# Performance work log

Hardware: AMD Instinct MI355X
Metric: run time of the kernel (lower is better)

Reference implementation:

```python
import jax, jax.numpy as jnp
import numpy as np

E, R, D, H = 8, 16, 2048, 8192
B, S = 2, 2048
SCALING = 2.0  # lora_alpha / r = 32 / 16


def gelu_new(x):
    # HF ACT2FN['gelu_new'] (tanh approximation), matches Phi config
    c = np.sqrt(2.0 / np.pi).astype(np.float32)
    return 0.5 * x * (1.0 + jnp.tanh(c * (x + 0.044715 * x * x * x)))


def _moe_lora(x, onehot, A, Bm):
    # x: [T,Din], A: [E,R,Din], Bm: [E,Dout,R], onehot: [T,E]
    # per-token low-rank projection for every expert (R is tiny), mask to the
    # assigned expert, then contract (e,r) jointly -> single [T,E*R]@[E*R,Dout] GEMM
    z = jnp.einsum('td,erd->ter', x, A) * onehot[:, :, None]  # [T,E,R]
    return jnp.einsum('ter,ehr->th', z, Bm)                   # [T,Dout]


def setup_inputs() -> dict:
    key = jax.random.key(0)
    ks = jax.random.split(key, 10)
    inv = lambda n: np.float32(1.0 / np.sqrt(n))
    return {
        'hidden_states': jax.random.normal(ks[0], (B, S, D), jnp.float32),
        'expert_idx': jax.random.randint(ks[1], (B, S), 0, E),
        'W1': jax.random.normal(ks[2], (H, D), jnp.float32) * inv(D),
        'b1': jax.random.normal(ks[3], (H,), jnp.float32) * 0.02,
        'A1': jax.random.normal(ks[4], (E, R, D), jnp.float32) * inv(D),
        'B1': jax.random.normal(ks[5], (E, H, R), jnp.float32) * 0.02,
        'W2': jax.random.normal(ks[6], (D, H), jnp.float32) * inv(H),
        'b2': jax.random.normal(ks[7], (D,), jnp.float32) * 0.02,
        'A2': jax.random.normal(ks[8], (E, R, H), jnp.float32) * inv(H),
        'B2': jax.random.normal(ks[9], (E, D, R), jnp.float32) * 0.02,
    }


def reference(hidden_states, expert_idx, W1, b1, A1, B1, W2, b2, A2, B2):
    b, s, d = hidden_states.shape
    x = hidden_states.reshape(b * s, d)                       # [T,D]
    onehot = jax.nn.one_hot(expert_idx.reshape(-1), A1.shape[0], dtype=x.dtype)
    # expert fc1: shared base layer + per-expert LoRA + shared bias
    h1 = x @ W1.T + b1 + SCALING * _moe_lora(x, onehot, A1, B1)
    y = gelu_new(h1)                                          # [T,H]
    # expert fc2
    out = y @ W2.T + b2 + SCALING * _moe_lora(y, onehot, A2, B2)
    return out.reshape(b, s, d)
```

## Files before the change

kernel.cpp:

```cpp
#include <hip/hip_runtime.h>
#include <hip/hip_bf16.h>
#include <math.h>

typedef __bf16 bf16_t;
typedef __bf16 bf16x4_t __attribute__((ext_vector_type(4)));
typedef __bf16 bf16x8_t __attribute__((ext_vector_type(8)));
typedef float  f32x4    __attribute__((ext_vector_type(4)));

#define NE  8
#define NR  16
#define ND  2048
#define NH  8192
#define NT  4096
#define NER 128
#define NK1 (ND + NER)
#define NK2 (NH + NER)

static __device__ __forceinline__ float gelu_fast(float x) {
    const float c2 = 1.5957691216057308f;
    float u2 = c2 * (x + 0.044715f * x * x * x);
    return x / (1.0f + __expf(-u2));
}

static __device__ __forceinline__ void load16_to_lds(const bf16_t* g, bf16_t* l) {
    __builtin_amdgcn_global_load_lds(
        (__attribute__((address_space(1))) void*)(g),
        (__attribute__((address_space(3))) void*)(l),
        16, 0, 0);
}

__global__ __launch_bounds__(256) void conv_x(
    const float* __restrict__ x, bf16_t* __restrict__ Xa1)
{
    const int i  = blockIdx.x * 256 + threadIdx.x;
    const int row = i >> 8;
    const int c8  = i & 255;
    f32x4 v0 = *(const f32x4*)(x + (long)i * 8);
    f32x4 v1 = *(const f32x4*)(x + (long)i * 8 + 4);
    bf16x8_t o = {(bf16_t)v0[0], (bf16_t)v0[1], (bf16_t)v0[2], (bf16_t)v0[3],
                  (bf16_t)v1[0], (bf16_t)v1[1], (bf16_t)v1[2], (bf16_t)v1[3]};
    *(bf16x8_t*)(Xa1 + (long)row * NK1 + (c8 << 3)) = o;
}

__global__ __launch_bounds__(256) void prep_main(
    const float* __restrict__ W, bf16_t* __restrict__ Waug,
    int ld, int shift8, int total8)
{
    const int i = blockIdx.x * 256 + threadIdx.x;
    if (i >= total8) return;
    const int row = i >> shift8;
    const int c8  = i & ((1 << shift8) - 1);
    f32x4 v0 = *(const f32x4*)(W + (long)i * 8);
    f32x4 v1 = *(const f32x4*)(W + (long)i * 8 + 4);
    bf16x8_t o = {(bf16_t)v0[0], (bf16_t)v0[1], (bf16_t)v0[2], (bf16_t)v0[3],
                  (bf16_t)v1[0], (bf16_t)v1[1], (bf16_t)v1[2], (bf16_t)v1[3]};
    *(bf16x8_t*)(Waug + (long)row * ld + (c8 << 3)) = o;
}

__global__ __launch_bounds__(256) void prep_lora(
    const float* __restrict__ Bl, bf16_t* __restrict__ Waug,
    int nrows, int K0, int ld, int total)
{
    const int i = blockIdx.x * 256 + threadIdx.x;
    if (i >= total) return;
    const int row = i >> 7;
    const int c   = i & 127;
    const int e   = c >> 4;
    const int r   = c & 15;
    float v = Bl[((long)e * nrows + row) * NR + r];
    Waug[(long)row * ld + K0 + c] = (bf16_t)v;
}

template <int SPLITS, int LD>
__global__ __launch_bounds__(256) void zred(
    const float* __restrict__ zp, const int* __restrict__ eidx,
    bf16_t* __restrict__ dst)
{
    const int i = blockIdx.x * 256 + threadIdx.x;
    const int t = i >> 7;
    const int c = i & 127;
    float s = 0.f;
#pragma unroll
    for (int j = 0; j < SPLITS; ++j) s += zp[(long)j * NT * 128 + i];
    const int e = eidx[t];
    float v = ((c >> 4) == e) ? 2.0f * s : 0.f;
    dst[(long)t * LD + c] = (bf16_t)v;
}

template <int BM, int BN, int W, int WM, int WN,
          int K, int LDA, int LDB, int LDC, int MODE>
__global__ __launch_bounds__(W * 64) void gemm_bt(
    const bf16_t* __restrict__ A,  const bf16_t* __restrict__ Bt,
    const float* __restrict__ bias, void* __restrict__ Cout)
{
    constexpr int RW  = BM / WM;
    constexpr int CW  = BN / WN;
    constexpr int MT  = RW / 16;
    constexpr int NTn = CW / 16;
    constexpr int AI  = BM / 16 / W;
    constexpr int BI  = BN / 16 / W;

    __shared__ union {
        struct { bf16_t As[2 * BM * 32]; bf16_t Bs[2 * BN * 32]; } s;
        bf16_t Cs[64 * 264];
    } u;

    const int tid   = threadIdx.x;
    const int wave  = tid >> 6;
    const int lane  = tid & 63;
    const int col16 = lane & 15;
    const int q     = lane >> 4;
    const int wm    = wave % WM;
    const int wn    = wave / WM;

    const int  rowA0 = blockIdx.y * BM;
    const int  colB0 = (MODE == 3) ? 0 : blockIdx.x * BN;
    const long koff  = (MODE == 3) ? (long)blockIdx.x * K : 0;

    const int srow  = lane >> 2;
    const int skoff = (lane & 3) * 8;

    const bf16_t* Agp[AI][2];
    const bf16_t* Bgp[BI][2];
    bf16_t*       AsD[AI][2];
    bf16_t*       BsD[BI][2];
#pragma unroll
    for (int jj = 0; jj < AI; ++jj) {
        const int j = (wave + jj * W) * 16;
#pragma unroll
        for (int h = 0; h < 2; ++h) {
            Agp[jj][h] = A + (long)(rowA0 + j + srow) * LDA + koff + h * 32 + skoff;
            AsD[jj][h] = &u.s.As[(h * BM + j) * 32];
        }
    }
#pragma unroll
    for (int jj = 0; jj < BI; ++jj) {
        const int j = (wave + jj * W) * 16;
#pragma unroll
        for (int h = 0; h < 2; ++h) {
            Bgp[jj][h] = Bt + (long)(colB0 + j + srow) * LDB + koff + h * 32 + skoff;
            BsD[jj][h] = &u.s.Bs[(h * BN + j) * 32];
        }
    }

    const bf16_t* Ard = &u.s.As[(wm * RW + col16) * 32 + q * 8];
    const bf16_t* Brd = &u.s.Bs[(wn * CW + col16) * 32 + q * 8];

    f32x4 acc[MT][NTn];
#pragma unroll
    for (int i = 0; i < MT; ++i)
#pragma unroll
        for (int j = 0; j < NTn; ++j)
            acc[i][j] = (f32x4){0.f, 0.f, 0.f, 0.f};

    for (int it = 0; it < K / 64; ++it) {
#pragma unroll
        for (int jj = 0; jj < AI; ++jj)
#pragma unroll
            for (int h = 0; h < 2; ++h) {
                load16_to_lds(Agp[jj][h], AsD[jj][h]);
                Agp[jj][h] += 64;
            }
#pragma unroll
        for (int jj = 0; jj < BI; ++jj)
#pragma unroll
            for (int h = 0; h < 2; ++h) {
                load16_to_lds(Bgp[jj][h], BsD[jj][h]);
                Bgp[jj][h] += 64;
            }
        __syncthreads();

#pragma unroll
        for (int h = 0; h < 2; ++h) {
            bf16x8_t af[MT], bfr[NTn];
#pragma unroll
            for (int mt = 0; mt < MT; ++mt)
                af[mt] = *(const bf16x8_t*)(Ard + (h * BM + mt * 16) * 32);
#pragma unroll
            for (int nt = 0; nt < NTn; ++nt)
                bfr[nt] = *(const bf16x8_t*)(Brd + (h * BN + nt * 16) * 32);
#pragma unroll
            for (int mt = 0; mt < MT; ++mt)
#pragma unroll
                for (int nt = 0; nt < NTn; ++nt)
                    acc[mt][nt] = __builtin_amdgcn_mfma_f32_16x16x32_bf16(
                        af[mt], bfr[nt], acc[mt][nt], 0, 0, 0);
        }
        __syncthreads();
    }

    if (MODE == 3) {
        float* Cf = (float*)Cout + (long)blockIdx.x * NT * LDC;
#pragma unroll
        for (int nt = 0; nt < NTn; ++nt) {
            const int col = wn * CW + nt * 16 + col16;
#pragma unroll
            for (int mt = 0; mt < MT; ++mt) {
                const int row0 = rowA0 + wm * RW + mt * 16 + q * 4;
#pragma unroll
                for (int i = 0; i < 4; ++i)
                    Cf[(long)(row0 + i) * LDC + col] = acc[mt][nt][i];
            }
        }
    }
}


#define BARRIER8() do { __builtin_amdgcn_sched_barrier(0); \
    __builtin_amdgcn_s_barrier(); \
    __builtin_amdgcn_sched_barrier(0); } while (0)

#define WAITLG8() do { asm volatile("s_waitcnt lgkmcnt(0)" ::: "memory"); \
    __builtin_amdgcn_sched_barrier(0); } while (0)

template <int N>
static __device__ __forceinline__ void wait_vm() {
    static_assert(N == 0 || N == 3 || N == 4, "unsupported vmcnt");
    if constexpr (N == 0) asm volatile("s_waitcnt vmcnt(0)" ::: "memory");
    if constexpr (N == 3) asm volatile("s_waitcnt vmcnt(3)" ::: "memory");
    if constexpr (N == 4) asm volatile("s_waitcnt vmcnt(4)" ::: "memory");
}

#define STAGE_A8(TT, KH) do { \
    char* ld_ = smem + (((((TT) & 1) << 1) + (KH)) * ASLOT) + sdW; \
    const bf16_t* g_ = gA + (long)(TT) * 64 + (KH) * 32; \
    _Pragma("unroll") \
    for (int j_ = 0; j_ < LA; ++j_) \
        load16_to_lds(g_ + (long)j_ * 128 * LDA_, (bf16_t*)(ld_ + j_ * 8192)); \
} while (0)

#define STAGE_B8(TT, KH) do { \
    char* ld_ = smem + BOFF0 + (((((TT) & 1) << 1) + (KH)) * BSLOT) + sdW; \
    const bf16_t* g_ = gB + (long)(TT) * 64 + (KH) * 32; \
    _Pragma("unroll") \
    for (int j_ = 0; j_ < LB; ++j_) \
        load16_to_lds(g_ + (long)j_ * 128 * LDB_, (bf16_t*)(ld_ + j_ * 8192)); \
} while (0)

#define RD_A8(RP, KH, MH) do { \
    const char* p_ = smem + (((RP) * 2 + (KH)) * ASLOT) \
                   + (wm * RW + (MH) * (RW / 2)) * 64 + rdoff; \
    _Pragma("unroll") \
    for (int mt_ = 0; mt_ < MT2; ++mt_) \
        af[mt_] = *(const bf16x8_t*)(p_ + mt_ * 1024); \
} while (0)

#define RD_B8(RP, KH) do { \
    const char* p_ = smem + BOFF0 + (((RP) * 2 + (KH)) * BSLOT) \
                   + (wn * CW) * 64 + rdoff; \
    _Pragma("unroll") \
    for (int nt_ = 0; nt_ < NTn; ++nt_) \
        bfr[nt_] = *(const bf16x8_t*)(p_ + nt_ * 1024); \
} while (0)

#define MFMA_PH8(MH) do { \
    __builtin_amdgcn_s_setprio(1); \
    _Pragma("unroll") \
    for (int mt_ = 0; mt_ < MT2; ++mt_) \
        _Pragma("unroll") \
        for (int nt_ = 0; nt_ < NTn; ++nt_) \
            acc[(MH) * MT2 + mt_][nt_] = __builtin_amdgcn_mfma_f32_16x16x32_bf16( \
                af[mt_], bfr[nt_], acc[(MH) * MT2 + mt_][nt_], 0, 0, 0); \
    __builtin_amdgcn_s_setprio(0); \
} while (0)

#define TILE8(T_, ST_) do { \
    const int rp_ = (T_) & 1; \
     \
    RD_A8(rp_, 0, 0); RD_B8(rp_, 0); \
    if (ST_) STAGE_A8((T_) + 1, 0); \
    BARRIER8(); WAITLG8(); MFMA_PH8(0); BARRIER8(); \
     \
    RD_A8(rp_, 0, 1); \
    if (ST_) { STAGE_B8((T_) + 1, 0); wait_vm<LA + LB>(); } \
    else     { wait_vm<0>(); } \
    BARRIER8(); WAITLG8(); MFMA_PH8(1); BARRIER8(); \
     \
    RD_A8(rp_, 1, 0); RD_B8(rp_, 1); \
    if (ST_) STAGE_A8((T_) + 1, 1); \
    BARRIER8(); WAITLG8(); MFMA_PH8(0); BARRIER8(); \
     \
    RD_A8(rp_, 1, 1); \
    if (ST_) { STAGE_B8((T_) + 1, 1); wait_vm<LA + LB>(); } \
    BARRIER8(); WAITLG8(); MFMA_PH8(1); BARRIER8(); \
} while (0)

template <int BN, int WM, int WN, int KT, int LDA_, int LDB_, int LDC_, int MODE>
__global__ __launch_bounds__(512, 2) void gemm8(
    const bf16_t* __restrict__ A, const bf16_t* __restrict__ Bt,
    const float* __restrict__ bias, void* __restrict__ Cout)
{
    constexpr int BM    = 256;
    constexpr int RW    = BM / WM;
    constexpr int CW    = BN / WN;
    constexpr int MT    = RW / 16;
    constexpr int MT2   = MT / 2;
    constexpr int NTn   = CW / 16;
    constexpr int LA    = 2;
    constexpr int LB    = BN / 128;
    constexpr int NTIL  = KT / 64;
    constexpr int ASLOT = 16384;
    constexpr int BSLOT = BN * 64;
    constexpr int BOFF0 = 4 * ASLOT;
    constexpr int RING  = BOFF0 + 4 * BSLOT;
    constexpr int CSB   = 64 * 264 * 2;
    constexpr int SMEM  = (MODE == 0 && CSB > RING) ? CSB : RING;

    __shared__ __align__(16) char smem[SMEM];

    const int tid   = threadIdx.x;
    const int wave  = tid >> 6;
    const int lane  = tid & 63;
    const int col16 = lane & 15;
    const int q     = lane >> 4;
    const int wm    = wave % WM;
    const int wn    = wave / WM;

    const int rowA0 = blockIdx.y * BM;
    const int colB0 = blockIdx.x * BN;

    const int srow = tid >> 2;
    const int sseg = (tid & 3) ^ ((tid >> 3) & 3);
    const bf16_t* gA = A  + (long)(rowA0 + srow) * LDA_ + sseg * 8;
    const bf16_t* gB = Bt + (long)(colB0 + srow) * LDB_ + sseg * 8;
    const int sdW = wave << 10;

    const int rdoff = col16 * 64 + ((q ^ ((lane >> 1) & 3)) << 4);

    bf16x8_t af[MT2];
    bf16x8_t bfr[NTn];
    f32x4 acc[MT][NTn];
#pragma unroll
    for (int i = 0; i < MT; ++i)
#pragma unroll
        for (int j = 0; j < NTn; ++j)
            acc[i][j] = (f32x4){0.f, 0.f, 0.f, 0.f};

    STAGE_A8(0, 0); STAGE_B8(0, 0); STAGE_A8(0, 1); STAGE_B8(0, 1);
    wait_vm<LA + LB>();
    BARRIER8();

    for (int t = 0; t < NTIL - 1; ++t) TILE8(t, 1);
    TILE8(NTIL - 1, 0);

    if (MODE == 1) {
        float* Cf = (float*)Cout;
#pragma unroll
        for (int nt = 0; nt < NTn; ++nt) {
            const int col = colB0 + wn * CW + nt * 16 + col16;
            const float bv = bias[col];
#pragma unroll
            for (int mt = 0; mt < MT; ++mt) {
                const int row0 = rowA0 + wm * RW + mt * 16 + q * 4;
#pragma unroll
                for (int i = 0; i < 4; ++i)
                    Cf[(long)(row0 + i) * LDC_ + col] = acc[mt][nt][i] + bv;
            }
        }
    } else {
        bf16_t* Cb = (bf16_t*)Cout;
        bf16_t* Cs = (bf16_t*)smem;
#pragma unroll
        for (int ph = 0; ph < BM / 64; ++ph) {
            const int phwm = (ph * 64) / RW;
            const int mtb  = ((ph * 64) % RW) / 16;
            if (wm == phwm) {
#pragma unroll
                for (int nt = 0; nt < NTn; ++nt) {
                    const int c = wn * CW + nt * 16 + col16;
                    const float bv = bias[colB0 + c];
#pragma unroll
                    for (int mt = 0; mt < 4; ++mt) {
                        const int rl = mt * 16 + q * 4;
#pragma unroll
                        for (int i = 0; i < 4; ++i)
                            Cs[(rl + i) * 264 + c] =
                                (bf16_t)gelu_fast(acc[mtb + mt][nt][i] + bv);
                    }
                }
            }
            __syncthreads();
            {
                constexpr int CPR = BN / 32;
                const int r  = tid / CPR;
                const int c0 = (tid % CPR) * 32;
                const long gbase =
                    (long)(rowA0 + ph * 64 + r) * LDC_ + colB0 + c0;
#pragma unroll
                for (int ch = 0; ch < 4; ++ch) {
                    bf16x8_t v = *(const bf16x8_t*)&Cs[r * 264 + c0 + ch * 8];
                    *(bf16x8_t*)&Cb[gbase + ch * 8] = v;
                }
            }
            __syncthreads();
        }
    }
}

extern "C" void kernel_launch(void* const* d_in, const int* in_sizes, int n_in,
                              void* d_out, int out_size, void* d_ws, size_t ws_size,
                              hipStream_t stream)
{
    const float* x    = (const float*)d_in[0];
    const int*   eidx = (const int*)  d_in[1];
    const float* W1   = (const float*)d_in[2];
    const float* b1   = (const float*)d_in[3];
    const float* A1   = (const float*)d_in[4];
    const float* B1   = (const float*)d_in[5];
    const float* W2   = (const float*)d_in[6];
    const float* b2   = (const float*)d_in[7];
    const float* A2   = (const float*)d_in[8];
    const float* B2   = (const float*)d_in[9];
    float* out = (float*)d_out;

    char* ws = (char*)d_ws;
    bf16_t* Xaug2 = (bf16_t*)(ws);
    bf16_t* Xaug1 = (bf16_t*)(ws + 68157440L);
    bf16_t* W1aug = (bf16_t*)(ws + 85983232L);
    bf16_t* W2aug = (bf16_t*)(ws + 68157440L);
    bf16_t* A1b   = (bf16_t*)(ws + 104000000L);
    bf16_t* A2b   = (bf16_t*)(ws + 104857600L);
    float*  zp1   = (float*) (ws + 106954752L);
    float*  zp2   = (float*) (ws + 85983232L);

    conv_x<<<NT * ND / 8 / 256, 256, 0, stream>>>(x, Xaug1);
    prep_main<<<(NER * ND / 8) / 256, 256, 0, stream>>>(A1, A1b, ND, 8, NER * ND / 8);
    {
        dim3 g(4, NT / 128);
        gemm_bt<128, 128, 4, 2, 2, 512, NK1, ND, 128, 3><<<g, 256, 0, stream>>>(
            Xaug1, A1b, nullptr, (void*)zp1);
    }
    zred<4, NK1><<<NT * 128 / 256, 256, 0, stream>>>(zp1, eidx, Xaug1 + ND);
    prep_main<<<(NH * ND / 8) / 256, 256, 0, stream>>>(W1, W1aug, NK1, 8, NH * ND / 8);
    prep_lora<<<(NH * NER) / 256, 256, 0, stream>>>(B1, W1aug, NH, ND, NK1, NH * NER);
    {
        dim3 g(NH / 256, NT / 256);
        gemm8<256, 2, 4, NK1, NK1, NK1, NK2, 0><<<g, 512, 0, stream>>>(
            Xaug1, W1aug, b1, (void*)Xaug2);
    }

    prep_main<<<(NER * NH / 8) / 256, 256, 0, stream>>>(A2, A2b, NH, 10, NER * NH / 8);
    {
        dim3 g(8, NT / 128);
        gemm_bt<128, 128, 4, 2, 2, 1024, NK2, NH, 128, 3><<<g, 256, 0, stream>>>(
            Xaug2, A2b, nullptr, (void*)zp2);
    }
    zred<8, NK2><<<NT * 128 / 256, 256, 0, stream>>>(zp2, eidx, Xaug2 + NH);
    prep_main<<<(ND * NH / 8) / 256, 256, 0, stream>>>(W2, W2aug, NK2, 10, ND * NH / 8);
    prep_lora<<<(ND * NER) / 256, 256, 0, stream>>>(B2, W2aug, ND, NH, NK2, ND * NER);
    {
        dim3 g(ND / 128, NT / 256);
        gemm8<128, 4, 2, NK2, NK2, NK2, ND, 1><<<g, 512, 0, stream>>>(
            Xaug2, W2aug, b2, (void*)out);
    }
}
```

Baseline: 550.9 us.

## Deepen GEMM K-pipeline prefetch and use inline-asm LDS reads with immediate offsets

Restructures the staged global-to-LDS pipeline so that parts of tile t+2 are prefetched while tile t is computed. Only the second A half of tile t+1 is left for the current iteration, and the vmcnt waits and prologue are adjusted to match. LDS fragment reads become explicit ds_read_b128 with immediate offsets, which cuts address arithmetic. The aim is to hide more global-load latency behind the MFMA work. In exchange it relies on slot reuse across the 2-deep ring being correct, and asm volatile reads may limit the compiler's scheduling.

```diff
diff --git a/kernel.cpp b/kernel.cpp
--- a/kernel.cpp
+++ b/kernel.cpp
@@ -6,6 +6,7 @@
 typedef __bf16 bf16x4_t __attribute__((ext_vector_type(4)));
 typedef __bf16 bf16x8_t __attribute__((ext_vector_type(8)));
 typedef float  f32x4    __attribute__((ext_vector_type(4)));
+typedef const __attribute__((address_space(3))) char* lds_cp;
 
 #define NE  8
 #define NR  16
@@ -27,6 +28,14 @@
         (__attribute__((address_space(1))) void*)(g),
         (__attribute__((address_space(3))) void*)(l),
         16, 0, 0);
+}
+
+template <int OFF>
+static __device__ __forceinline__ bf16x8_t ds_read_b128_o(lds_cp p) {
+    bf16x8_t r;
+    asm volatile("ds_read_b128 %0, %1 offset:%2"
+                 : "=v"(r) : "v"(p), "i"(OFF));
+    return r;
 }
 
 __global__ __launch_bounds__(256) void conv_x(
@@ -215,10 +224,10 @@
 
 template <int N>
 static __device__ __forceinline__ void wait_vm() {
-    static_assert(N == 0 || N == 3 || N == 4, "unsupported vmcnt");
+    static_assert(N == 0 || N == 4 || N == 6, "unsupported vmcnt");
     if constexpr (N == 0) asm volatile("s_waitcnt vmcnt(0)" ::: "memory");
-    if constexpr (N == 3) asm volatile("s_waitcnt vmcnt(3)" ::: "memory");
     if constexpr (N == 4) asm volatile("s_waitcnt vmcnt(4)" ::: "memory");
+    if constexpr (N == 6) asm volatile("s_waitcnt vmcnt(6)" ::: "memory");
 }
 
 #define STAGE_A8(TT, KH) do { \
@@ -238,19 +247,23 @@
 } while (0)
 
 #define RD_A8(RP, KH, MH) do { \
-    const char* p_ = smem + (((RP) * 2 + (KH)) * ASLOT) \
-                   + (wm * RW + (MH) * (RW / 2)) * 64 + rdoff; \
-    _Pragma("unroll") \
-    for (int mt_ = 0; mt_ < MT2; ++mt_) \
-        af[mt_] = *(const bf16x8_t*)(p_ + mt_ * 1024); \
+    lds_cp p_ = sb3 + (((RP) * 2 + (KH)) * ASLOT) \
+              + (wm * RW + (MH) * (RW / 2)) * 64 + rdoff; \
+    af[0] = ds_read_b128_o<0>(p_); \
+    af[1] = ds_read_b128_o<1024>(p_); \
+    if constexpr (MT2 > 2) { \
+        af[2] = ds_read_b128_o<2048>(p_); \
+        af[3] = ds_read_b128_o<3072>(p_); \
+    } \
 } while (0)
 
 #define RD_B8(RP, KH) do { \
-    const char* p_ = smem + BOFF0 + (((RP) * 2 + (KH)) * BSLOT) \
-                   + (wn * CW) * 64 + rdoff; \
-    _Pragma("unroll") \
-    for (int nt_ = 0; nt_ < NTn; ++nt_) \
-        bfr[nt_] = *(const bf16x8_t*)(p_ + nt_ * 1024); \
+    lds_cp p_ = sb3 + BOFF0 + (((RP) * 2 + (KH)) * BSLOT) \
+              + (wn * CW) * 64 + rdoff; \
+    bfr[0] = ds_read_b128_o<0>(p_); \
+    bfr[1] = ds_read_b128_o<1024>(p_); \
+    bfr[2] = ds_read_b128_o<2048>(p_); \
+    bfr[3] = ds_read_b128_o<3072>(p_); \
 } while (0)
 
 #define MFMA_PH8(MH) do { \
@@ -268,20 +281,20 @@
     const int rp_ = (T_) & 1; \
      \
     RD_A8(rp_, 0, 0); RD_B8(rp_, 0); \
-    if (ST_) STAGE_A8((T_) + 1, 0); \
+    if (ST_ >= 1) STAGE_A8((T_) + 1, 1); \
     BARRIER8(); WAITLG8(); MFMA_PH8(0); BARRIER8(); \
      \
     RD_A8(rp_, 0, 1); \
-    if (ST_) { STAGE_B8((T_) + 1, 0); wait_vm<LA + LB>(); } \
-    else     { wait_vm<0>(); } \
+    if (ST_ == 2) STAGE_B8((T_) + 2, 0); \
     BARRIER8(); WAITLG8(); MFMA_PH8(1); BARRIER8(); \
      \
     RD_A8(rp_, 1, 0); RD_B8(rp_, 1); \
-    if (ST_) STAGE_A8((T_) + 1, 1); \
+    if (ST_ == 2) STAGE_A8((T_) + 2, 0); \
     BARRIER8(); WAITLG8(); MFMA_PH8(0); BARRIER8(); \
      \
     RD_A8(rp_, 1, 1); \
-    if (ST_) { STAGE_B8((T_) + 1, 1); wait_vm<LA + LB>(); } \
+    if (ST_ == 2) { STAGE_B8((T_) + 2, 1); wait_vm<NV>(); } \
+    else if (ST_ == 1) { wait_vm<0>(); } \
     BARRIER8(); WAITLG8(); MFMA_PH8(1); BARRIER8(); \
 } while (0)
 
@@ -298,7 +311,9 @@
     constexpr int NTn   = CW / 16;
     constexpr int LA    = 2;
     constexpr int LB    = BN / 128;
+    constexpr int NV    = LA + 2 * LB;
     constexpr int NTIL  = KT / 64;
+    static_assert(NTIL >= 3, "need >=3 K-tiles");
     constexpr int ASLOT = 16384;
     constexpr int BSLOT = BN * 64;
     constexpr int BOFF0 = 4 * ASLOT;
@@ -326,6 +341,7 @@
     const int sdW = wave << 10;
 
     const int rdoff = col16 * 64 + ((q ^ ((lane >> 1) & 3)) << 4);
+    lds_cp sb3 = (lds_cp)smem;
 
     bf16x8_t af[MT2];
     bf16x8_t bfr[NTn];
@@ -337,10 +353,12 @@
             acc[i][j] = (f32x4){0.f, 0.f, 0.f, 0.f};
 
     STAGE_A8(0, 0); STAGE_B8(0, 0); STAGE_A8(0, 1); STAGE_B8(0, 1);
-    wait_vm<LA + LB>();
+    STAGE_A8(1, 0); STAGE_B8(1, 0); STAGE_B8(1, 1);
+    wait_vm<NV>();
     BARRIER8();
 
-    for (int t = 0; t < NTIL - 1; ++t) TILE8(t, 1);
+    for (int t = 0; t < NTIL - 2; ++t) TILE8(t, 2);
+    TILE8(NTIL - 2, 1);
     TILE8(NTIL - 1, 0);
 
     if (MODE == 1) {
```

New measurement: 555.4 us. About the same (+0.8%).

## Deepen GEMM K-pipeline with staggered half-tile prefetch and lighter barriers

Applied to the files above, without the earlier changes.

Restructures the GEMM main loop so global-to-LDS staging runs further ahead: slot halves are refilled as soon as their data has been consumed, with a staggered prologue and a two-tile unrolled loop using pointer increments. It also drops the explicit sched_barrier fences and lgkmcnt waits around barriers, which frees the compiler to interleave LDS reads with MFMA. The goal is to hide more global-load latency and cut scheduling stalls. In exchange, correctness now depends on the compiler inserting the right LDS waits and on the reworked vmcnt accounting.

```diff
diff --git a/kernel.cpp b/kernel.cpp
--- a/kernel.cpp
+++ b/kernel.cpp
@@ -206,54 +206,49 @@
 }
 
 
-#define BARRIER8() do { __builtin_amdgcn_sched_barrier(0); \
-    __builtin_amdgcn_s_barrier(); \
-    __builtin_amdgcn_sched_barrier(0); } while (0)
-
-#define WAITLG8() do { asm volatile("s_waitcnt lgkmcnt(0)" ::: "memory"); \
-    __builtin_amdgcn_sched_barrier(0); } while (0)
+#define BAR8() __builtin_amdgcn_s_barrier()
 
 template <int N>
 static __device__ __forceinline__ void wait_vm() {
-    static_assert(N == 0 || N == 3 || N == 4, "unsupported vmcnt");
+    static_assert(N == 0 || N == 4 || N == 6, "unsupported vmcnt");
     if constexpr (N == 0) asm volatile("s_waitcnt vmcnt(0)" ::: "memory");
-    if constexpr (N == 3) asm volatile("s_waitcnt vmcnt(3)" ::: "memory");
     if constexpr (N == 4) asm volatile("s_waitcnt vmcnt(4)" ::: "memory");
-}
-
-#define STAGE_A8(TT, KH) do { \
-    char* ld_ = smem + (((((TT) & 1) << 1) + (KH)) * ASLOT) + sdW; \
-    const bf16_t* g_ = gA + (long)(TT) * 64 + (KH) * 32; \
+    if constexpr (N == 6) asm volatile("s_waitcnt vmcnt(6)" ::: "memory");
+}
+
+#define STG_A(P_, KH, TE) do { \
+    char* ld_ = smem + (((P_) * 2 + (KH)) * ASLOT) + sdW; \
+    const bf16_t* g_ = gA + (TE); \
     _Pragma("unroll") \
     for (int j_ = 0; j_ < LA; ++j_) \
         load16_to_lds(g_ + (long)j_ * 128 * LDA_, (bf16_t*)(ld_ + j_ * 8192)); \
 } while (0)
 
-#define STAGE_B8(TT, KH) do { \
-    char* ld_ = smem + BOFF0 + (((((TT) & 1) << 1) + (KH)) * BSLOT) + sdW; \
-    const bf16_t* g_ = gB + (long)(TT) * 64 + (KH) * 32; \
+#define STG_B(P_, KH, TE) do { \
+    char* ld_ = smem + BOFF0 + (((P_) * 2 + (KH)) * BSLOT) + sdW; \
+    const bf16_t* g_ = gB + (TE); \
     _Pragma("unroll") \
     for (int j_ = 0; j_ < LB; ++j_) \
         load16_to_lds(g_ + (long)j_ * 128 * LDB_, (bf16_t*)(ld_ + j_ * 8192)); \
 } while (0)
 
-#define RD_A8(RP, KH, MH) do { \
-    const char* p_ = smem + (((RP) * 2 + (KH)) * ASLOT) \
+#define RD_A(P_, KH, MH) do { \
+    const char* p_ = smem + (((P_) * 2 + (KH)) * ASLOT) \
                    + (wm * RW + (MH) * (RW / 2)) * 64 + rdoff; \
     _Pragma("unroll") \
     for (int mt_ = 0; mt_ < MT2; ++mt_) \
         af[mt_] = *(const bf16x8_t*)(p_ + mt_ * 1024); \
 } while (0)
 
-#define RD_B8(RP, KH) do { \
-    const char* p_ = smem + BOFF0 + (((RP) * 2 + (KH)) * BSLOT) \
+#define RD_B(P_, KH) do { \
+    const char* p_ = smem + BOFF0 + (((P_) * 2 + (KH)) * BSLOT) \
                    + (wn * CW) * 64 + rdoff; \
     _Pragma("unroll") \
     for (int nt_ = 0; nt_ < NTn; ++nt_) \
         bfr[nt_] = *(const bf16x8_t*)(p_ + nt_ * 1024); \
 } while (0)
 
-#define MFMA_PH8(MH) do { \
+#define MFMA_C(MH) do { \
     __builtin_amdgcn_s_setprio(1); \
     _Pragma("unroll") \
     for (int mt_ = 0; mt_ < MT2; ++mt_) \
@@ -264,25 +259,24 @@
     __builtin_amdgcn_s_setprio(0); \
 } while (0)
 
-#define TILE8(T_, ST_) do { \
-    const int rp_ = (T_) & 1; \
+#define TILE(RP, TO, ST) do { \
      \
-    RD_A8(rp_, 0, 0); RD_B8(rp_, 0); \
-    if (ST_) STAGE_A8((T_) + 1, 0); \
-    BARRIER8(); WAITLG8(); MFMA_PH8(0); BARRIER8(); \
+    RD_A(RP, 0, 0); RD_B(RP, 0); \
+    if (ST >= 1) STG_A(RP ^ 1, 1, (TO) + 96); \
+    BAR8(); MFMA_C(0); BAR8(); \
      \
-    RD_A8(rp_, 0, 1); \
-    if (ST_) { STAGE_B8((T_) + 1, 0); wait_vm<LA + LB>(); } \
-    else     { wait_vm<0>(); } \
-    BARRIER8(); WAITLG8(); MFMA_PH8(1); BARRIER8(); \
+    RD_A(RP, 0, 1); \
+    if (ST == 2) STG_B(RP, 0, (TO) + 128); \
+    BAR8(); MFMA_C(1); BAR8(); \
      \
-    RD_A8(rp_, 1, 0); RD_B8(rp_, 1); \
-    if (ST_) STAGE_A8((T_) + 1, 1); \
-    BARRIER8(); WAITLG8(); MFMA_PH8(0); BARRIER8(); \
+    RD_A(RP, 1, 0); RD_B(RP, 1); \
+    if (ST == 2) STG_A(RP, 0, (TO) + 128); \
+    BAR8(); MFMA_C(0); BAR8(); \
      \
-    RD_A8(rp_, 1, 1); \
-    if (ST_) { STAGE_B8((T_) + 1, 1); wait_vm<LA + LB>(); } \
-    BARRIER8(); WAITLG8(); MFMA_PH8(1); BARRIER8(); \
+    RD_A(RP, 1, 1); \
+    if (ST == 2) { STG_B(RP, 1, (TO) + 160); wait_vm<NV>(); } \
+    else if (ST == 1) { wait_vm<0>(); } \
+    BAR8(); MFMA_C(1); BAR8(); \
 } while (0)
 
 template <int BN, int WM, int WN, int KT, int LDA_, int LDB_, int LDC_, int MODE>
@@ -298,7 +292,9 @@
     constexpr int NTn   = CW / 16;
     constexpr int LA    = 2;
     constexpr int LB    = BN / 128;
+    constexpr int NV    = LA + 2 * LB;
     constexpr int NTIL  = KT / 64;
+    static_assert(NTIL >= 4 && (NTIL & 1) == 0, "need even NTIL >= 4");
     constexpr int ASLOT = 16384;
     constexpr int BSLOT = BN * 64;
     constexpr int BOFF0 = 4 * ASLOT;
@@ -336,12 +332,19 @@
         for (int j = 0; j < NTn; ++j)
             acc[i][j] = (f32x4){0.f, 0.f, 0.f, 0.f};
 
-    STAGE_A8(0, 0); STAGE_B8(0, 0); STAGE_A8(0, 1); STAGE_B8(0, 1);
-    wait_vm<LA + LB>();
-    BARRIER8();
-
-    for (int t = 0; t < NTIL - 1; ++t) TILE8(t, 1);
-    TILE8(NTIL - 1, 0);
+    STG_A(0, 0, 0);  STG_B(0, 0, 0);  STG_A(0, 1, 32); STG_B(0, 1, 32);
+    STG_A(1, 0, 64); STG_B(1, 0, 64); STG_B(1, 1, 96);
+    wait_vm<NV>();
+    BAR8();
+
+    for (int i = 0; i < (NTIL - 2) / 2; ++i) {
+        TILE(0, 0, 2);
+        TILE(1, 64, 2);
+        gA += 128;
+        gB += 128;
+    }
+    TILE(0, 0, 1);
+    TILE(1, 64, 0);
 
     if (MODE == 1) {
         float* Cf = (float*)Cout;
```

Measured after the change: 555.3 us. Within noise of the previous version (+0.8%).
